# Performance work log

Measured on AMD Instinct MI355X. Metric: run time of the kernel, lower is better.

Reference implementation:

```python
import jax, jax.numpy as jnp
import numpy as np

B, T, H, IN = 128, 2048, 200, 1  # batch, encoder len, hidden, decoder input feature
N_STEPS = 5


def setup_inputs() -> dict:
    key = jax.random.key(0)
    ks = jax.random.split(key, 16)
    g = lambda i, shape, s=0.05: (jax.random.normal(ks[i], shape, jnp.float32) * s)
    return {
        "x": g(0, (B, 1, IN), 1.0),
        "h0": g(1, (1, B, H), 1.0),
        "c0": g(2, (1, B, H), 1.0),
        "encoder_output": g(3, (B, T, H), 1.0),
        "Wa": g(4, (H, H)), "ba": jnp.zeros((H,), jnp.float32),
        "Ua": g(5, (H, H)), "bua": jnp.zeros((H,), jnp.float32),
        "Va": g(6, (1, H)), "bva": jnp.zeros((1,), jnp.float32),
        "W_ih": g(7, (4 * H, IN + H)), "W_hh": g(8, (4 * H, H)),
        "b_ih": jnp.zeros((4 * H,), jnp.float32), "b_hh": jnp.zeros((4 * H,), jnp.float32),
        "W1": g(9, (100, H)), "b1": jnp.zeros((100,), jnp.float32),
        "W2": g(10, (50, 100)), "b2": jnp.zeros((50,), jnp.float32),
        "W3": g(11, (1, 50)), "b3": jnp.zeros((1,), jnp.float32),
    }


def reference(x, h0, c0, encoder_output, Wa, ba, Ua, bua, Va, bva,
              W_ih, W_hh, b_ih, b_hh, W1, b1, W2, b2, W3, b3):
    # --- Bahdanau attention (query = h0 is constant across all 5 steps) ---
    q = h0[0]  # [B, H]
    q_proj = q @ Wa.T + ba                         # [B, H]
    k_proj = encoder_output @ Ua.T + bua           # [B, T, H]
    e = jnp.tanh(q_proj[:, None, :] + k_proj)      # [B, T, H]
    scores = e @ Va[0] + bva[0]                    # [B, T]
    attn = jax.nn.softmax(scores, axis=-1)         # [B, T]
    context = jnp.einsum("bt,bth->bh", attn, encoder_output)  # [B, H]

    c_prev = c0[0]                                 # [B, H] (constant each step)
    h_pre = q @ W_hh.T + b_hh                      # recurrent gate term, constant

    def step(x_t, _):
        # x_t: [B, IN]; LSTM input = cat(x, context) along features
        inp = jnp.concatenate([x_t, context], axis=-1)        # [B, IN+H]
        gates = inp @ W_ih.T + b_ih + h_pre                   # [B, 4H]
        i, f, g, o = jnp.split(gates, 4, axis=-1)             # torch gate order i,f,g,o
        c_new = jax.nn.sigmoid(f) * c_prev + jax.nn.sigmoid(i) * jnp.tanh(g)
        h_new = jax.nn.sigmoid(o) * jnp.tanh(c_new)
        out = jax.nn.relu(h_new)
        out = jax.nn.relu(out @ W1.T + b1)
        out = jax.nn.relu(out @ W2.T + b2)
        y = out @ W3.T + b3                                   # [B, 1]
        return y, y  # decoded output feeds back as next input

    _, ys = jax.lax.scan(step, x.reshape(B, IN), xs=None, length=N_STEPS)  # [5, B, 1]
    return jnp.transpose(ys[:, :, 0], (1, 0))  # [B, 5]
```

## Files before the change

kernel.cpp:

```cpp
#include <hip/hip_runtime.h>
#include <math.h>

#define B 128
#define T 2048
#define H 200
#define G4 800
#define KP 224
#define ESTR 208
#define ROWS 32

typedef short short8 __attribute__((ext_vector_type(8)));
typedef float floatx4 __attribute__((ext_vector_type(4)));

__device__ __forceinline__ unsigned short f2bf(float x) {
    unsigned u = __float_as_uint(x);
    return (unsigned short)((u + 0x7fffu + ((u >> 16) & 1u)) >> 16);
}
__device__ __forceinline__ float bf2f(unsigned short s) {
    return __uint_as_float(((unsigned)s) << 16);
}
__device__ __forceinline__ unsigned pk2(float a, float b) {
    return __builtin_amdgcn_perm(__float_as_uint(b) + 0x8000u,
                                 __float_as_uint(a) + 0x8000u, 0x07060302u);
}
__device__ __forceinline__ float ftanh(float x) {
    float e = __builtin_amdgcn_exp2f(x * 2.885390081777927f);
    float r = __builtin_amdgcn_rcpf(e + 1.f);
    return fmaf(-2.f, r, 1.f);
}
__device__ __forceinline__ float sigm(float x) { return 1.f / (1.f + expf(-x)); }

__global__ __launch_bounds__(256) void prep_all(const float* __restrict__ Ua,
                                                const float* __restrict__ Wa,
                                                const float* __restrict__ ba,
                                                const float* __restrict__ bua,
                                                const float* __restrict__ h0,
                                                const float* __restrict__ W_ih,
                                                const float* __restrict__ W_hh,
                                                const float* __restrict__ W1,
                                                const float* __restrict__ W2,
                                                unsigned short* __restrict__ Uab,
                                                float* __restrict__ WihT,
                                                float* __restrict__ WhhT,
                                                float* __restrict__ wx,
                                                float* __restrict__ qb,
                                                float* __restrict__ W1T,
                                                float* __restrict__ W2T) {
    __shared__ __align__(16) float qs[H];
    int bx = blockIdx.x, tid = threadIdx.x;
    if (bx < 256) {
        if (tid < KP) {
            float v = (bx < H && tid < H) ? Ua[bx * H + tid] : 0.f;
            Uab[bx * KP + tid] = f2bf(v);
        }
    } else if (bx < 456) {
        int k = bx - 256;
        for (int j = tid; j < G4; j += 256) WihT[k * G4 + j] = W_ih[(size_t)j * (H + 1) + 1 + k];
    } else if (bx < 656) {
        int k = bx - 456;
        for (int j = tid; j < G4; j += 256) WhhT[k * G4 + j] = W_hh[(size_t)j * H + k];
    } else if (bx == 656) {
        for (int j = tid; j < G4; j += 256) wx[j] = W_ih[(size_t)j * (H + 1)];
    } else if (bx < 785) {
        int b = bx - 657;
        if (tid < H) qs[tid] = h0[b * H + tid];
        __syncthreads();
        if (tid < H) {
            float a = ba[tid] + bua[tid];
            const float4* w  = (const float4*)(Wa + tid * H);
            const float4* qv = (const float4*)qs;
            #pragma unroll 8
            for (int k = 0; k < 50; k++) {
                float4 wv = w[k], q4 = qv[k];
                a = fmaf(wv.x, q4.x, a);
                a = fmaf(wv.y, q4.y, a);
                a = fmaf(wv.z, q4.z, a);
                a = fmaf(wv.w, q4.w, a);
            }
            qb[b * H + tid] = a;
        }
    } else if (bx < 985) {
        int k = bx - 785;
        if (tid < 100) W1T[k * 100 + tid] = W1[tid * H + k];
    } else {
        int k = bx - 985;
        if (tid < 50) W2T[k * 50 + tid] = W2[tid * 100 + k];
    }
}


template<int NM>
__device__ __forceinline__ void migscore(const unsigned short* __restrict__ Uab,
                                         const unsigned short* elds,
                                         const float* s_va, const float* s_qb,
                                         int m0, int r, int q, float p[2]) {
    short8 af[NM][7];
    #pragma unroll
    for (int m = 0; m < NM; m++)
        #pragma unroll
        for (int ks = 0; ks < 7; ks++)
            af[m][ks] = *(const short8*)(Uab + ((m0 + m) * 16 + r) * KP + ks * 32 + q * 8);
    #pragma unroll
    for (int nt = 0; nt < 2; nt++) {
        const unsigned short* rowp = elds + (nt * 16 + r) * ESTR;
        floatx4 C[NM];
        #pragma unroll
        for (int m = 0; m < NM; m++) C[m] = (floatx4){0.f, 0.f, 0.f, 0.f};
        #pragma unroll
        for (int ks = 0; ks < 7; ks++) {
            short8 bf = *(const short8*)(rowp + ks * 32 + q * 8);
            #pragma unroll
            for (int m = 0; m < NM; m++)
                C[m] = __builtin_amdgcn_mfma_f32_16x16x32_bf16(af[m][ks], bf, C[m], 0, 0, 0);
        }
        float pp = 0.f;
        #pragma unroll
        for (int m = 0; m < NM; m++)
            #pragma unroll
            for (int g = 0; g < 4; g++) {
                int h = (m0 + m) * 16 + q * 4 + g;
                pp += s_va[h] * ftanh(s_qb[h] + C[m][g]);
            }
        p[nt] += pp;
    }
}

__device__ __forceinline__ void stg(unsigned short* elds, int f, float4 v) {
    int row = f / 50, c4 = f - row * 50;
    uint2 wv;
    wv.x = pk2(v.x, v.y);
    wv.y = pk2(v.z, v.w);
    *(uint2*)&elds[row * ESTR + c4 * 4] = wv;
}

__global__ __launch_bounds__(256, 6) void scores_ctx(const float* __restrict__ enc,
                                                     const unsigned short* __restrict__ Uab,
                                                     const float* __restrict__ qb,
                                                     const float* __restrict__ Va,
                                                     const float* __restrict__ bva,
                                                     float* __restrict__ ctx_raw,
                                                     float* __restrict__ lsum) {
    __shared__ unsigned short elds[ROWS * ESTR + 32];
    __shared__ float s_qb[ESTR];
    __shared__ float s_va[ESTR];
    __shared__ float part[4][ROWS];
    __shared__ float wlds[ROWS];

    int bx  = blockIdx.x;
    int b   = bx >> 6;
    int t0  = (bx & 63) * ROWS;
    int tid = threadIdx.x, w = tid >> 6, lane = tid & 63, r = lane & 15, q = lane >> 4;

    const float4* gsrc = (const float4*)(enc + (size_t)(b * T + t0) * H);

    float4 a0 = gsrc[tid];
    float4 a1 = gsrc[tid + 256];
    float4 a2 = gsrc[tid + 512];

    if (tid < 200) { s_qb[tid] = qb[b * H + tid]; s_va[tid] = Va[tid]; }
    else if (tid < 208) { s_qb[tid] = 0.f; s_va[tid] = 0.f; }
    float bv = bva[0];

    if (tid < 128) {
        int row = tid >> 2, pr = tid & 3;
        *(unsigned*)&elds[row * ESTR + 200 + pr * 2] = 0u;
    } else if (tid < 144) {
        *(unsigned*)&elds[ROWS * ESTR + (tid - 128) * 2] = 0u;
    }

    stg(elds, tid,       a0);
    stg(elds, tid + 256, a1);
    stg(elds, tid + 512, a2);
    __builtin_amdgcn_sched_barrier(0);

    float4 b0 = gsrc[tid + 768];
    float4 b1 = gsrc[tid + 1024];
    float4 b2 = gsrc[tid + 1280];
    float4 b3;
    if (tid < 64) b3 = gsrc[tid + 1536];
    stg(elds, tid + 768,  b0);
    stg(elds, tid + 1024, b1);
    stg(elds, tid + 1280, b2);
    if (tid < 64) stg(elds, tid + 1536, b3);
    __syncthreads();

    float p[2] = {0.f, 0.f};
    if (w == 0) {
        migscore<2>(Uab, elds, s_va, s_qb, 0, r, q, p);
        migscore<2>(Uab, elds, s_va, s_qb, 2, r, q, p);
    } else {
        int mb = 1 + 3 * w;
        migscore<2>(Uab, elds, s_va, s_qb, mb, r, q, p);
        migscore<1>(Uab, elds, s_va, s_qb, mb + 2, r, q, p);
    }
    #pragma unroll
    for (int nt = 0; nt < 2; nt++) {
        float pp = p[nt];
        pp += __shfl_xor(pp, 16);
        pp += __shfl_xor(pp, 32);
        if (q == 0) part[w][nt * 16 + r] = pp;
    }
    __syncthreads();

    if (w == 0) {
        float a = fabsf(s_va[lane]) + fabsf(s_va[lane + 64]) + fabsf(s_va[lane + 128]);
        if (lane < 16) a += fabsf(s_va[lane + 192]);
        #pragma unroll
        for (int d = 1; d < 64; d <<= 1) a += __shfl_xor(a, d);
        float bound = a + fabsf(bv);

        float we = 0.f;
        if (lane < ROWS) {
            float s = part[0][lane] + part[1][lane] + part[2][lane] + part[3][lane] + bv;
            we = __builtin_amdgcn_exp2f((s - bound) * 1.4426950408889634f);
            wlds[lane] = we;
        }
        #pragma unroll
        for (int d = 1; d < 64; d <<= 1) we += __shfl_xor(we, d);
        if (lane == 0) atomicAdd(&lsum[b], we);
    }
    __syncthreads();

    if (tid < H) {
        float a0c = 0.f, a1c = 0.f, a2c = 0.f, a3c = 0.f;
        #pragma unroll
        for (int t = 0; t < ROWS; t += 4) {
            a0c = fmaf(wlds[t],     bf2f(elds[(t    ) * ESTR + tid]), a0c);
            a1c = fmaf(wlds[t + 1], bf2f(elds[(t + 1) * ESTR + tid]), a1c);
            a2c = fmaf(wlds[t + 2], bf2f(elds[(t + 2) * ESTR + tid]), a2c);
            a3c = fmaf(wlds[t + 3], bf2f(elds[(t + 3) * ESTR + tid]), a3c);
        }
        atomicAdd(&ctx_raw[b * H + tid], (a0c + a1c) + (a2c + a3c));
    }
}

__global__ __launch_bounds__(512) void decoder2(const float* __restrict__ x,
                                                const float* __restrict__ c0,
                                                const float* __restrict__ ctx_raw,
                                                const float* __restrict__ lsum,
                                                const float* __restrict__ h0,
                                                const float* __restrict__ WihT,
                                                const float* __restrict__ WhhT,
                                                const float* __restrict__ b_ih,
                                                const float* __restrict__ b_hh,
                                                const float* __restrict__ wx,
                                                const float* __restrict__ W1T,
                                                const float* __restrict__ b1,
                                                const float* __restrict__ W2T,
                                                const float* __restrict__ b2,
                                                const float* __restrict__ W3,
                                                const float* __restrict__ b3,
                                                float* __restrict__ out) {
    __shared__ float s_gc[G4];
    __shared__ float s_wx[G4];
    __shared__ float s_ctx[H];
    __shared__ float s_q[H];
    __shared__ float s_out[H];
    __shared__ float s_o1[100];
    __shared__ float s_o2[50];
    __shared__ float s_w3[64];
    __shared__ float s_x;
    int b = blockIdx.x, tid = threadIdx.x;

    if (tid < H) {
        float invl = 1.f / lsum[b];
        s_ctx[tid] = ctx_raw[b * H + tid] * invl;
        s_q[tid]   = h0[b * H + tid];
    }
    s_wx[tid] = wx[tid];
    if (tid < G4 - 512) s_wx[512 + tid] = wx[512 + tid];
    if (tid < 64) s_w3[tid] = (tid < 50) ? W3[tid] : 0.f;
    if (tid == 0) s_x = x[b];
    float b3v = b3[0];
    __syncthreads();

    {
        int j0 = tid;
        int j1 = 512 + ((tid < 288) ? tid : 287);
        float a0 = b_ih[j0] + b_hh[j0];
        float a1 = b_ih[j1] + b_hh[j1];
        #pragma unroll 4
        for (int k = 0; k < H; k++) {
            float cv = s_ctx[k], qv = s_q[k];
            a0 = fmaf(cv, WihT[k * G4 + j0], a0);
            a0 = fmaf(qv, WhhT[k * G4 + j0], a0);
            a1 = fmaf(cv, WihT[k * G4 + j1], a1);
            a1 = fmaf(qv, WhhT[k * G4 + j1], a1);
        }
        s_gc[j0] = a0;
        if (tid < 288) s_gc[512 + tid] = a1;
    }
    float cprev = (tid < H) ? c0[b * H + tid] : 0.f;
    __syncthreads();

    for (int s = 0; s < 5; s++) {
        float xv = s_x;
        if (tid < H) {
            float ig = s_gc[tid]         + xv * s_wx[tid];
            float fg = s_gc[H + tid]     + xv * s_wx[H + tid];
            float gg = s_gc[2 * H + tid] + xv * s_wx[2 * H + tid];
            float og = s_gc[3 * H + tid] + xv * s_wx[3 * H + tid];
            float c  = sigm(fg) * cprev + sigm(ig) * tanhf(gg);
            float hn = sigm(og) * tanhf(c);
            s_out[tid] = fmaxf(hn, 0.f);
        }
        __syncthreads();
        if (tid < 400) {
            int j = tid >> 2, q4 = tid & 3;
            float a = 0.f;
            const float* wp = W1T + (q4 * 50) * 100 + j;
            const float* op = s_out + q4 * 50;
            #pragma unroll 10
            for (int k = 0; k < 50; k++) a = fmaf(wp[k * 100], op[k], a);
            a += __shfl_xor(a, 1);
            a += __shfl_xor(a, 2);
            if (q4 == 0) s_o1[j] = fmaxf(a + b1[j], 0.f);
        }
        __syncthreads();
        if (tid < 200) {
            int j = tid >> 2, q4 = tid & 3;
            float a = 0.f;
            const float* wp = W2T + (q4 * 25) * 50 + j;
            const float* op = s_o1 + q4 * 25;
            #pragma unroll 5
            for (int k = 0; k < 25; k++) a = fmaf(wp[k * 50], op[k], a);
            a += __shfl_xor(a, 1);
            a += __shfl_xor(a, 2);
            if (q4 == 0) s_o2[j] = fmaxf(a + b2[j], 0.f);
        }
        __syncthreads();
        if (tid < 64) {
            float a = (tid < 50) ? s_w3[tid] * s_o2[tid] : 0.f;
            #pragma unroll
            for (int d = 1; d < 64; d <<= 1) a += __shfl_xor(a, d);
            if (tid == 0) {
                float y = a + b3v;
                out[b * 5 + s] = y;
                s_x = y;
            }
        }
        __syncthreads();
    }
}

extern "C" void kernel_launch(void* const* d_in, const int* in_sizes, int n_in,
                              void* d_out, int out_size, void* d_ws, size_t ws_size,
                              hipStream_t stream) {
    (void)in_sizes; (void)n_in; (void)out_size; (void)ws_size;
    const float* x    = (const float*)d_in[0];
    const float* h0   = (const float*)d_in[1];
    const float* c0   = (const float*)d_in[2];
    const float* enc  = (const float*)d_in[3];
    const float* Wa   = (const float*)d_in[4];
    const float* ba   = (const float*)d_in[5];
    const float* Ua   = (const float*)d_in[6];
    const float* bua  = (const float*)d_in[7];
    const float* Va   = (const float*)d_in[8];
    const float* bva  = (const float*)d_in[9];
    const float* W_ih = (const float*)d_in[10];
    const float* W_hh = (const float*)d_in[11];
    const float* b_ih = (const float*)d_in[12];
    const float* b_hh = (const float*)d_in[13];
    const float* W1   = (const float*)d_in[14];
    const float* b1   = (const float*)d_in[15];
    const float* W2   = (const float*)d_in[16];
    const float* b2   = (const float*)d_in[17];
    const float* W3   = (const float*)d_in[18];
    const float* b3   = (const float*)d_in[19];
    float* out = (float*)d_out;

    char* ws = (char*)d_ws;
    unsigned short* Uab = (unsigned short*)(ws);
    float* WihT    = (float*)(ws + 114688);
    float* WhhT    = (float*)(ws + 754688);
    float* wx      = (float*)(ws + 1394688);
    float* qb      = (float*)(ws + 1397888);
    float* W1T     = (float*)(ws + 1500288);
    float* W2T     = (float*)(ws + 1580288);
    float* ctx_raw = (float*)(ws + 1600288);
    float* lsum    = (float*)(ws + 1702688);

    hipMemsetAsync(ws + 1600288, 0, 102912, stream);
    prep_all<<<dim3(1085), 256, 0, stream>>>(Ua, Wa, ba, bua, h0, W_ih, W_hh, W1, W2,
                                             Uab, WihT, WhhT, wx, qb, W1T, W2T);
    scores_ctx<<<dim3(8192), 256, 0, stream>>>(enc, Uab, qb, Va, bva, ctx_raw, lsum);
    decoder2<<<dim3(B), 512, 0, stream>>>(x, c0, ctx_raw, lsum, h0, WihT, WhhT,
                                          b_ih, b_hh, wx, W1T, b1, W2T, b2, W3, b3, out);
}
```

Before: 172.6 us.

## Double encoder rows per scores block to reuse Ua fragments across more tiles

Each scores_ctx block now processes 64 encoder timesteps instead of 32, halving the grid to 4096 blocks. The per-wave Ua bf16 fragments loaded from global memory are reused across four 16-row MFMA tiles instead of two, which halves the weight reloads and the per-block atomics into ctx and lsum. The LDS row stride goes from 208 to 216, presumably to change bank mapping, and occupancy is lowered to 4 blocks per SM to fit the larger LDS tile and more registers. Loading more data before compute can expose more memory latency per block.

Measured after the change: 177.7 us. +3.0%, slower.

```diff
diff --git a/kernel.cpp b/kernel.cpp
--- a/kernel.cpp
+++ b/kernel.cpp
@@ -6,8 +6,8 @@
 #define H 200
 #define G4 800
 #define KP 224
-#define ESTR 208
-#define ROWS 32
+#define ESTR 216
+#define ROWS 64
 
 typedef short short8 __attribute__((ext_vector_type(8)));
 typedef float floatx4 __attribute__((ext_vector_type(4)));
@@ -93,7 +93,7 @@
 __device__ __forceinline__ void migscore(const unsigned short* __restrict__ Uab,
                                          const unsigned short* elds,
                                          const float* s_va, const float* s_qb,
-                                         int m0, int r, int q, float p[2]) {
+                                         int m0, int r, int q, float p[4]) {
     short8 af[NM][7];
     #pragma unroll
     for (int m = 0; m < NM; m++)
@@ -101,7 +101,7 @@
         for (int ks = 0; ks < 7; ks++)
             af[m][ks] = *(const short8*)(Uab + ((m0 + m) * 16 + r) * KP + ks * 32 + q * 8);
     #pragma unroll
-    for (int nt = 0; nt < 2; nt++) {
+    for (int nt = 0; nt < 4; nt++) {
         const unsigned short* rowp = elds + (nt * 16 + r) * ESTR;
         floatx4 C[NM];
         #pragma unroll
@@ -133,22 +133,22 @@
     *(uint2*)&elds[row * ESTR + c4 * 4] = wv;
 }
 
-__global__ __launch_bounds__(256, 6) void scores_ctx(const float* __restrict__ enc,
+__global__ __launch_bounds__(256, 4) void scores_ctx(const float* __restrict__ enc,
                                                      const unsigned short* __restrict__ Uab,
                                                      const float* __restrict__ qb,
                                                      const float* __restrict__ Va,
                                                      const float* __restrict__ bva,
                                                      float* __restrict__ ctx_raw,
                                                      float* __restrict__ lsum) {
-    __shared__ unsigned short elds[ROWS * ESTR + 32];
-    __shared__ float s_qb[ESTR];
-    __shared__ float s_va[ESTR];
+    __shared__ unsigned short elds[ROWS * ESTR + 16];
+    __shared__ float s_qb[208];
+    __shared__ float s_va[208];
     __shared__ float part[4][ROWS];
     __shared__ float wlds[ROWS];
 
     int bx  = blockIdx.x;
-    int b   = bx >> 6;
-    int t0  = (bx & 63) * ROWS;
+    int b   = bx >> 5;
+    int t0  = (bx & 31) * ROWS;
     int tid = threadIdx.x, w = tid >> 6, lane = tid & 63, r = lane & 15, q = lane >> 4;
 
     const float4* gsrc = (const float4*)(enc + (size_t)(b * T + t0) * H);
@@ -156,35 +156,49 @@
     float4 a0 = gsrc[tid];
     float4 a1 = gsrc[tid + 256];
     float4 a2 = gsrc[tid + 512];
+    float4 a3 = gsrc[tid + 768];
+    float4 a4 = gsrc[tid + 1024];
+    float4 a5 = gsrc[tid + 1280];
 
     if (tid < 200) { s_qb[tid] = qb[b * H + tid]; s_va[tid] = Va[tid]; }
     else if (tid < 208) { s_qb[tid] = 0.f; s_va[tid] = 0.f; }
     float bv = bva[0];
 
-    if (tid < 128) {
-        int row = tid >> 2, pr = tid & 3;
-        *(unsigned*)&elds[row * ESTR + 200 + pr * 2] = 0u;
-    } else if (tid < 144) {
-        *(unsigned*)&elds[ROWS * ESTR + (tid - 128) * 2] = 0u;
-    }
-
-    stg(elds, tid,       a0);
-    stg(elds, tid + 256, a1);
-    stg(elds, tid + 512, a2);
+    {
+        int i0 = tid, i1 = tid + 256;
+        int row0 = i0 >> 3, pr0 = i0 & 7;
+        int row1 = i1 >> 3, pr1 = i1 & 7;
+        *(unsigned*)&elds[row0 * ESTR + 200 + pr0 * 2] = 0u;
+        *(unsigned*)&elds[row1 * ESTR + 200 + pr1 * 2] = 0u;
+        if (tid < 8) *(unsigned*)&elds[ROWS * ESTR + tid * 2] = 0u;
+    }
+
+    stg(elds, tid,        a0);
+    stg(elds, tid + 256,  a1);
+    stg(elds, tid + 512,  a2);
+    stg(elds, tid + 768,  a3);
+    stg(elds, tid + 1024, a4);
+    stg(elds, tid + 1280, a5);
     __builtin_amdgcn_sched_barrier(0);
 
-    float4 b0 = gsrc[tid + 768];
-    float4 b1 = gsrc[tid + 1024];
-    float4 b2 = gsrc[tid + 1280];
-    float4 b3;
-    if (tid < 64) b3 = gsrc[tid + 1536];
-    stg(elds, tid + 768,  b0);
-    stg(elds, tid + 1024, b1);
-    stg(elds, tid + 1280, b2);
-    if (tid < 64) stg(elds, tid + 1536, b3);
+    float4 b0 = gsrc[tid + 1536];
+    float4 b1 = gsrc[tid + 1792];
+    float4 b2 = gsrc[tid + 2048];
+    float4 b3 = gsrc[tid + 2304];
+    float4 b4 = gsrc[tid + 2560];
+    float4 b5 = gsrc[tid + 2816];
+    float4 c0;
+    if (tid < 128) c0 = gsrc[tid + 3072];
+    stg(elds, tid + 1536, b0);
+    stg(elds, tid + 1792, b1);
+    stg(elds, tid + 2048, b2);
+    stg(elds, tid + 2304, b3);
+    stg(elds, tid + 2560, b4);
+    stg(elds, tid + 2816, b5);
+    if (tid < 128) stg(elds, tid + 3072, c0);
     __syncthreads();
 
-    float p[2] = {0.f, 0.f};
+    float p[4] = {0.f, 0.f, 0.f, 0.f};
     if (w == 0) {
         migscore<2>(Uab, elds, s_va, s_qb, 0, r, q, p);
         migscore<2>(Uab, elds, s_va, s_qb, 2, r, q, p);
@@ -194,7 +208,7 @@
         migscore<1>(Uab, elds, s_va, s_qb, mb + 2, r, q, p);
     }
     #pragma unroll
-    for (int nt = 0; nt < 2; nt++) {
+    for (int nt = 0; nt < 4; nt++) {
         float pp = p[nt];
         pp += __shfl_xor(pp, 16);
         pp += __shfl_xor(pp, 32);
@@ -209,12 +223,9 @@
         for (int d = 1; d < 64; d <<= 1) a += __shfl_xor(a, d);
         float bound = a + fabsf(bv);
 
-        float we = 0.f;
-        if (lane < ROWS) {
-            float s = part[0][lane] + part[1][lane] + part[2][lane] + part[3][lane] + bv;
-            we = __builtin_amdgcn_exp2f((s - bound) * 1.4426950408889634f);
-            wlds[lane] = we;
-        }
+        float s  = part[0][lane] + part[1][lane] + part[2][lane] + part[3][lane] + bv;
+        float we = __builtin_amdgcn_exp2f((s - bound) * 1.4426950408889634f);
+        wlds[lane] = we;
         #pragma unroll
         for (int d = 1; d < 64; d <<= 1) we += __shfl_xor(we, d);
         if (lane == 0) atomicAdd(&lsum[b], we);
@@ -223,7 +234,7 @@
 
     if (tid < H) {
         float a0c = 0.f, a1c = 0.f, a2c = 0.f, a3c = 0.f;
-        #pragma unroll
+        #pragma unroll 4
         for (int t = 0; t < ROWS; t += 4) {
             a0c = fmaf(wlds[t],     bf2f(elds[(t    ) * ESTR + tid]), a0c);
             a1c = fmaf(wlds[t + 1], bf2f(elds[(t + 1) * ESTR + tid]), a1c);
@@ -383,7 +394,7 @@
     hipMemsetAsync(ws + 1600288, 0, 102912, stream);
     prep_all<<<dim3(1085), 256, 0, stream>>>(Ua, Wa, ba, bua, h0, W_ih, W_hh, W1, W2,
                                              Uab, WihT, WhhT, wx, qb, W1T, W2T);
-    scores_ctx<<<dim3(8192), 256, 0, stream>>>(enc, Uab, qb, Va, bva, ctx_raw, lsum);
+    scores_ctx<<<dim3(4096), 256, 0, stream>>>(enc, Uab, qb, Va, bva, ctx_raw, lsum);
     decoder2<<<dim3(B), 512, 0, stream>>>(x, c0, ctx_raw, lsum, h0, WihT, WhhT,
                                           b_ih, b_hh, wx, W1T, b1, W2T, b2, W3, b3, out);
 }
```
